# Performance work log

Measured on AMD Instinct MI355X. Metric: run time of the kernel, lower is better.

Reference implementation:

```python
import jax, jax.numpy as jnp
import numpy as np

B, T, D = 8, 1024, 1024
H, HD, KVH, R = 16, 64, 4, 256   # heads, head_dim, kv_heads, kv_lora_rank
K = 31                            # depthwise conv kernel
FF = 4 * D
EPS = 1e-5


def _ln(x, g, b):
    m = jnp.mean(x, -1, keepdims=True)
    v = jnp.mean((x - m) ** 2, -1, keepdims=True)
    return (x - m) * jax.lax.rsqrt(v + EPS) * g + b


def _rope_tables(seq, dim):
    inv = 1.0 / (10000.0 ** (np.arange(0, dim, 2, dtype=np.float32) / dim))
    t = np.arange(seq, dtype=np.float32)
    f = np.einsum('i,j->ij', t, inv)
    emb = np.concatenate([f, f], -1)
    return jnp.asarray(np.cos(emb)), jnp.asarray(np.sin(emb))


def _rope(x, cos, sin):
    # x: [B, h, T, HD]; cos/sin: [T, HD]
    x1, x2 = jnp.split(x, 2, axis=-1)
    return x * cos + jnp.concatenate([-x2, x1], -1) * sin


def setup_inputs() -> dict:
    key = jax.random.key(0)
    ks = iter(jax.random.split(key, 48))
    def w(shape, s=0.02):
        return jax.random.normal(next(ks), shape, jnp.float32) * s
    d = {}
    d['x'] = jax.random.normal(next(ks), (B, T, D), jnp.float32)
    d['ff1_ng'] = jnp.ones(D); d['ff1_nb'] = jnp.zeros(D)
    d['ff1_w1'] = w((D, FF)); d['ff1_b1'] = jnp.zeros(FF)
    d['ff1_w2'] = w((FF, D)); d['ff1_b2'] = jnp.zeros(D)
    d['attn_ng'] = jnp.ones(D); d['attn_nb'] = jnp.zeros(D)
    d['wq'] = w((D, H * HD)); d['wkva'] = w((D, R + HD))
    d['kvn_g'] = jnp.ones(R); d['kvn_b'] = jnp.zeros(R)
    d['wkvb'] = w((R, KVH * HD * 2)); d['wo'] = w((H * HD, D))
    d['conv_ng'] = jnp.ones(D); d['conv_nb'] = jnp.zeros(D)
    d['pw1_w'] = w((D, 2 * D)); d['pw1_b'] = jnp.zeros(2 * D)
    d['dw_w'] = w((D, 1, K)); d['dw_b'] = jnp.zeros(D)
    d['bn_g'] = jnp.ones(D); d['bn_b'] = jnp.zeros(D)
    d['bn_rm'] = jnp.zeros(D); d['bn_rv'] = jnp.ones(D)
    d['pw2_w'] = w((D, D)); d['pw2_b'] = jnp.zeros(D)
    d['ff2_ng'] = jnp.ones(D); d['ff2_nb'] = jnp.zeros(D)
    d['ff2_w1'] = w((D, FF)); d['ff2_b1'] = jnp.zeros(FF)
    d['ff2_w2'] = w((FF, D)); d['ff2_b2'] = jnp.zeros(D)
    d['fin_g'] = jnp.ones(D); d['fin_b'] = jnp.zeros(D)
    return d


def _ffn(x, ng, nb, w1, b1, w2, b2):
    h = jax.nn.silu(_ln(x, ng, nb) @ w1 + b1)
    return h @ w2 + b2


def _rmla(x, ng, nb, wq, wkva, kvn_g, kvn_b, wkvb, wo):
    h = _ln(x, ng, nb)
    q = (h @ wq).reshape(B, T, H, HD).transpose(0, 2, 1, 3)
    kva = h @ wkva                                  # [B,T,R+HD]; k_pe part unused (as in source)
    lat = _ln(kva[..., :R], kvn_g, kvn_b)
    kv = lat @ wkvb
    k = kv[..., :KVH * HD].reshape(B, T, KVH, HD).transpose(0, 2, 1, 3)
    v = kv[..., KVH * HD:].reshape(B, T, KVH, HD).transpose(0, 2, 1, 3)
    cos, sin = _rope_tables(T, HD)
    q = _rope(q, cos, sin)
    k = _rope(k, cos, sin)
    g = H // KVH
    k = jnp.repeat(k, g, axis=1)
    v = jnp.repeat(v, g, axis=1)
    s = jnp.einsum('bhqd,bhkd->bhqk', q, k) * (HD ** -0.5)
    a = jax.nn.softmax(s.astype(jnp.float32), axis=-1).astype(q.dtype)
    o = jnp.einsum('bhqk,bhkd->bhqd', a, v)
    o = o.transpose(0, 2, 1, 3).reshape(B, T, H * HD)
    return o @ wo


def _convmod(x, ng, nb, pw1_w, pw1_b, dw_w, dw_b, bn_g, bn_b, bn_rm, bn_rv, pw2_w, pw2_b):
    h = _ln(x, ng, nb)
    h = h @ pw1_w + pw1_b                           # [B,T,2D]
    a, gate = jnp.split(h, 2, axis=-1)
    h = a * jax.nn.sigmoid(gate)                    # GLU over channels
    h = h.transpose(0, 2, 1)                        # [B,D,T]
    h = jax.lax.conv_general_dilated(h, dw_w, (1,), [(K // 2, K // 2)],
                                     dimension_numbers=('NCH', 'OIH', 'NCH'),
                                     feature_group_count=D) + dw_b[None, :, None]
    h = (h - bn_rm[None, :, None]) * jax.lax.rsqrt(bn_rv[None, :, None] + EPS)
    h = h * bn_g[None, :, None] + bn_b[None, :, None]
    h = jax.nn.silu(h)
    h = h.transpose(0, 2, 1)                        # [B,T,D]
    return h @ pw2_w + pw2_b


def reference(x, ff1_ng, ff1_nb, ff1_w1, ff1_b1, ff1_w2, ff1_b2,
              attn_ng, attn_nb, wq, wkva, kvn_g, kvn_b, wkvb, wo,
              conv_ng, conv_nb, pw1_w, pw1_b, dw_w, dw_b, bn_g, bn_b, bn_rm, bn_rv, pw2_w, pw2_b,
              ff2_ng, ff2_nb, ff2_w1, ff2_b1, ff2_w2, ff2_b2, fin_g, fin_b):
    # Conformer block (macaron): half-FF, RMLA attention, gated depthwise conv, half-FF, final LN
    x = x + 0.5 * _ffn(x, ff1_ng, ff1_nb, ff1_w1, ff1_b1, ff1_w2, ff1_b2)
    x = x + _rmla(x, attn_ng, attn_nb, wq, wkva, kvn_g, kvn_b, wkvb, wo)
    x = x + _convmod(x, conv_ng, conv_nb, pw1_w, pw1_b, dw_w, dw_b, bn_g, bn_b, bn_rm, bn_rv, pw2_w, pw2_b)
    x = x + 0.5 * _ffn(x, ff2_ng, ff2_nb, ff2_w1, ff2_b1, ff2_w2, ff2_b2)
    return _ln(x, fin_g, fin_b)
```

## Files before the change

kernel.cpp:

```cpp
#include <hip/hip_runtime.h>
#include <stdint.h>

typedef unsigned short u16;
using bf16x8 = __attribute__((ext_vector_type(8))) __bf16;
using f32x4  = __attribute__((ext_vector_type(4))) float;

__device__ __forceinline__ u16 f2bf(float f) {
    uint32_t u = __float_as_uint(f);
    u += 0x7fffu + ((u >> 16) & 1u);
    return (u16)(u >> 16);
}
__device__ __forceinline__ float bf2f(u16 u) {
    return __uint_as_float(((uint32_t)u) << 16);
}
__device__ __forceinline__ void gload16(const void* g, void* l) {
    __builtin_amdgcn_global_load_lds(
        (__attribute__((address_space(1))) void*)(uintptr_t)g,
        (__attribute__((address_space(3))) void*)(uintptr_t)l,
        16, 0, 0);
}

template <int OUTF32>
__global__ __launch_bounds__(256) void ln_kernel(const float* __restrict__ in,
                                                 const float* __restrict__ g,
                                                 const float* __restrict__ b,
                                                 void* __restrict__ out, int D) {
    const int row = blockIdx.x;
    const int tid = threadIdx.x;
    const float* x = in + (size_t)row * D;
    const int nv = D >> 8;
    float v[4];
    float s1 = 0.f, s2 = 0.f;
    for (int i = 0; i < nv; ++i) {
        float t = x[tid + (i << 8)];
        v[i] = t; s1 += t; s2 += t * t;
    }
    for (int o = 1; o < 64; o <<= 1) {
        s1 += __shfl_xor(s1, o, 64);
        s2 += __shfl_xor(s2, o, 64);
    }
    __shared__ float r1[4], r2[4];
    const int w = tid >> 6;
    if ((tid & 63) == 0) { r1[w] = s1; r2[w] = s2; }
    __syncthreads();
    s1 = r1[0] + r1[1] + r1[2] + r1[3];
    s2 = r2[0] + r2[1] + r2[2] + r2[3];
    const float mean = s1 / (float)D;
    const float var  = s2 / (float)D - mean * mean;
    const float inv  = rsqrtf(var + 1e-5f);
    for (int i = 0; i < nv; ++i) {
        int c = tid + (i << 8);
        float y = (v[i] - mean) * inv * g[c] + b[c];
        if (OUTF32) ((float*)out)[(size_t)row * D + c] = y;
        else        ((u16*)out)[(size_t)row * D + c] = f2bf(y);
    }
}

template <int GLUPERM>
__global__ __launch_bounds__(256) void wconvert_t(const float* __restrict__ W,
                                                  u16* __restrict__ Wt,
                                                  int K, int N, int ldw) {
    __shared__ float tile[32][33];
    const int k0 = blockIdx.x * 32, n0 = blockIdx.y * 32;
    const int tx = threadIdx.x & 31, ty = threadIdx.x >> 5;
    const int csrc = GLUPERM ? ((tx & 1) * 1024 + (n0 >> 1) + (tx >> 1)) : (n0 + tx);
    for (int i = 0; i < 4; ++i)
        tile[ty + i * 8][tx] = W[(size_t)(k0 + ty + i * 8) * ldw + csrc];
    __syncthreads();
    for (int i = 0; i < 4; ++i)
        Wt[(size_t)(n0 + ty + i * 8) * K + k0 + tx] = f2bf(tile[tx][ty + i * 8]);
}

template <int EPI>
__global__ __launch_bounds__(256) void gemm_bf16(const u16* __restrict__ A,
                                                 const u16* __restrict__ Bt,
                                                 const float* __restrict__ bias,
                                                 const float* __restrict__ res,
                                                 float rscale,
                                                 void* __restrict__ outp,
                                                 int M, int N, int K, int nbx) {
    __shared__ u16 sA[128 * 64];
    __shared__ u16 sB[128 * 64];
    const int tid = threadIdx.x;
    const int lane = tid & 63;
    const int w = tid >> 6;
    const int wm = w >> 1, wn = w & 1;
    const int fr = lane & 15, fq = lane >> 4, frx = fr & 7;
    const int cpx = gridDim.x >> 3;
    const int lid = (blockIdx.x & 7) * cpx + (blockIdx.x >> 3);
    const int bn0 = (lid % nbx) * 128;
    const int bm0 = (lid / nbx) * 128;

    f32x4 acc[4][4] = {};

    const int lrow = lane >> 3;
    const int lslot = (lane & 7) ^ lrow;
    const u16* ga0 = A  + (size_t)(bm0 + w * 8 + lrow) * K + lslot * 8;
    const u16* gb0 = Bt + (size_t)(bn0 + w * 8 + lrow) * K + lslot * 8;
    u16* la0 = sA + w * 512;
    u16* lb0 = sB + w * 512;
    const size_t rstep32 = (size_t)32 * K;

    for (int kt = 0; kt < K; kt += 64) {
        __syncthreads();
#pragma unroll
        for (int i = 0; i < 4; ++i) {
            gload16(ga0 + kt + i * rstep32, la0 + i * 2048);
            gload16(gb0 + kt + i * rstep32, lb0 + i * 2048);
        }
        __syncthreads();
#pragma unroll
        for (int kk = 0; kk < 2; ++kk) {
            bf16x8 afr[4], bfr[4];
            const int sl = (((kk * 4 + fq) ^ frx) << 3);
#pragma unroll
            for (int i = 0; i < 4; ++i) {
                afr[i] = *(const bf16x8*)(sA + (wm * 64 + i * 16 + fr) * 64 + sl);
                bfr[i] = *(const bf16x8*)(sB + (wn * 64 + i * 16 + fr) * 64 + sl);
            }
#pragma unroll
            for (int mi = 0; mi < 4; ++mi)
#pragma unroll
                for (int ni = 0; ni < 4; ++ni)
                    acc[mi][ni] = __builtin_amdgcn_mfma_f32_16x16x32_bf16(
                        bfr[ni], afr[mi], acc[mi][ni], 0, 0, 0);
        }
    }

#pragma unroll
    for (int mi = 0; mi < 4; ++mi) {
        const int m = bm0 + wm * 64 + mi * 16 + fr;
#pragma unroll
        for (int ni = 0; ni < 4; ++ni) {
            const int n0 = bn0 + wn * 64 + ni * 16 + fq * 4;
            if (EPI == 0 || EPI == 1) {
                union { uint2 u2; u16 hh[4]; } ok;
#pragma unroll
                for (int r = 0; r < 4; ++r) {
                    float v = acc[mi][ni][r] + (bias ? bias[n0 + r] : 0.f);
                    if (EPI == 1) v = v / (1.f + __expf(-v));
                    ok.hh[r] = f2bf(v);
                }
                *(uint2*)((u16*)outp + (size_t)m * N + n0) = ok.u2;
            } else if (EPI == 2) {
                f32x4 v;
#pragma unroll
                for (int r = 0; r < 4; ++r)
                    v[r] = acc[mi][ni][r] + (bias ? bias[n0 + r] : 0.f);
                *(f32x4*)((float*)outp + (size_t)m * N + n0) = v;
            } else if (EPI == 3) {
                const f32x4 rv = *(const f32x4*)(res + (size_t)m * N + n0);
                f32x4 v;
#pragma unroll
                for (int r = 0; r < 4; ++r)
                    v[r] = rv[r] + rscale * (acc[mi][ni][r] + (bias ? bias[n0 + r] : 0.f));
                *(f32x4*)((float*)outp + (size_t)m * N + n0) = v;
            } else {
                float vv[4];
#pragma unroll
                for (int r = 0; r < 4; ++r) {
                    const int n = n0 + r;
                    vv[r] = acc[mi][ni][r] + bias[((n & 1) << 10) + (n >> 1)];
                }
                union { uint32_t u; u16 hh[2]; } ok;
                ok.hh[0] = f2bf(vv[0] / (1.f + __expf(-vv[1])));
                ok.hh[1] = f2bf(vv[2] / (1.f + __expf(-vv[3])));
                *(uint32_t*)((u16*)outp + (size_t)m * (N >> 1) + (n0 >> 1)) = ok.u;
            }
        }
    }
}

__global__ __launch_bounds__(256) void rope_tables_kernel(float* __restrict__ ct,
                                                          float* __restrict__ st) {
    const int i = blockIdx.x * 256 + threadIdx.x;
    const int t = i >> 5, j = i & 31;
    const float inv = powf(10000.f, -(float)j / 32.f);
    const float f = (float)t * inv;
    ct[i] = cosf(f);
    st[i] = sinf(f);
}

__global__ __launch_bounds__(256) void rope_kernel(u16* __restrict__ buf,
                                                   const float* __restrict__ ct,
                                                   const float* __restrict__ st,
                                                   int hmask, int hshift, int rstride,
                                                   float scale) {
    const int i = blockIdx.x * 256 + threadIdx.x;
    const int j = i & 31;
    const int hh = (i >> 5) & hmask;
    const int m = i >> (5 + hshift);
    const int t = m & 1023;
    u16* p = buf + (size_t)m * rstride + hh * 64 + j;
    const float c = ct[t * 32 + j], s = st[t * 32 + j];
    const float x1 = bf2f(p[0]), x2 = bf2f(p[32]);
    p[0]  = f2bf((x1 * c - x2 * s) * scale);
    p[32] = f2bf((x2 * c + x1 * s) * scale);
}

__global__ __launch_bounds__(256) void vtranspose_kernel(const u16* __restrict__ KV,
                                                         u16* __restrict__ Vt) {
    __shared__ u16 tile[32][33];
    const int t0 = blockIdx.x * 32, h0 = blockIdx.y * 32;
    const int bk = blockIdx.z;
    const int b = bk >> 2, kh = bk & 3;
    const int tx = threadIdx.x & 31, ty = threadIdx.x >> 5;
    for (int i = 0; i < 4; ++i)
        tile[ty + i * 8][tx] =
            KV[(size_t)(b * 1024 + t0 + ty + i * 8) * 512 + 256 + kh * 64 + h0 + tx];
    __syncthreads();
    for (int i = 0; i < 4; ++i)
        Vt[((size_t)bk * 64 + h0 + ty + i * 8) * 1024 + t0 + tx] = tile[tx][ty + i * 8];
}

__global__ __launch_bounds__(256) void attn_kernel(const u16* __restrict__ Q,
                                                   const u16* __restrict__ KV,
                                                   const u16* __restrict__ Vt,
                                                   u16* __restrict__ O) {
    __shared__ __align__(16) u16 sK[2][64 * 64];
    __shared__ __align__(16) u16 sV[2][64 * 64];
    __shared__ __align__(16) u16 sP[4][16 * 64];
    const int tid = threadIdx.x, lane = tid & 63, w = tid >> 6;
    const int fr = lane & 15, fq = lane >> 4, frx = fr & 7;
    const int bk = blockIdx.x, b = bk >> 2, kh = bk & 3;
    const int h = kh * 4 + w;
    const int q0 = blockIdx.y * 16;
    const int qrow = b * 1024 + q0 + fr;

    const int srow = w * 16 + (lane >> 3);
    const int sslot = (lane & 7) ^ ((lane >> 3) & 7);
    const u16* gK = KV + (size_t)(b * 1024 + srow) * 512 + kh * 64 + sslot * 8;
    const u16* gV = Vt + (size_t)((b * 4 + kh) * 64 + srow) * 1024 + sslot * 8;
    u16* dK = (u16*)sK + w * 16 * 64;
    u16* dV = (u16*)sV + w * 16 * 64;

    bf16x8 qf[2];
    qf[0] = *(const bf16x8*)(Q + (size_t)qrow * 1024 + h * 64 + fq * 8);
    qf[1] = *(const bf16x8*)(Q + (size_t)qrow * 1024 + h * 64 + 32 + fq * 8);

    f32x4 oacc[4] = {};
    float mrun = -1e30f, lrun = 0.f;
    u16* sPw = sP[w];

    gload16(gK, dK);
    gload16(gK + (size_t)8 * 512, dK + 8 * 64);
    gload16(gV, dV);
    gload16(gV + (size_t)8 * 1024, dV + 8 * 64);
    __syncthreads();

    int cur = 0;
    for (int t = 0; t < 16; ++t) {
        const int kv0 = t * 64;
        if (t < 15) {
            const int kn = kv0 + 64;
            const int nx = (cur ^ 1) * 4096;
            gload16(gK + (size_t)kn * 512,       dK + nx);
            gload16(gK + (size_t)(kn + 8) * 512, dK + nx + 8 * 64);
            gload16(gV + kn,                     dV + nx);
            gload16(gV + kn + (size_t)8 * 1024,  dV + nx + 8 * 64);
        }
        const u16* sKc = (u16*)sK + cur * 4096;
        const u16* sVc = (u16*)sV + cur * 4096;
        f32x4 sacc[4] = {};
#pragma unroll
        for (int ks = 0; ks < 2; ++ks)
#pragma unroll
            for (int nb = 0; nb < 4; ++nb) {
                const bf16x8 kf = *(const bf16x8*)(
                    sKc + (nb * 16 + fr) * 64 + (((ks * 4 + fq) ^ frx) << 3));
                sacc[nb] = __builtin_amdgcn_mfma_f32_16x16x32_bf16(kf, qf[ks], sacc[nb], 0, 0, 0);
            }
        float pm;
        {
            float a0 = fmaxf(fmaxf(sacc[0][0], sacc[0][1]), fmaxf(sacc[0][2], sacc[0][3]));
            float a1 = fmaxf(fmaxf(sacc[1][0], sacc[1][1]), fmaxf(sacc[1][2], sacc[1][3]));
            float a2 = fmaxf(fmaxf(sacc[2][0], sacc[2][1]), fmaxf(sacc[2][2], sacc[2][3]));
            float a3 = fmaxf(fmaxf(sacc[3][0], sacc[3][1]), fmaxf(sacc[3][2], sacc[3][3]));
            pm = fmaxf(fmaxf(a0, a1), fmaxf(a2, a3));
        }
        pm = fmaxf(pm, __shfl_xor(pm, 16, 64));
        pm = fmaxf(pm, __shfl_xor(pm, 32, 64));
        if (!__all(pm <= mrun + 8.f)) {
            const float mn = fmaxf(mrun, pm);
            const float al = __expf(mrun - mn);
            mrun = mn;
            lrun *= al;
#pragma unroll
            for (int f = 0; f < 4; ++f) {
                f32x4 tt = oacc[f];
#pragma unroll
                for (int r = 0; r < 4; ++r) tt[r] *= al;
                oacc[f] = tt;
            }
        }
        float rs = 0.f;
#pragma unroll
        for (int nb = 0; nb < 4; ++nb) {
            union { uint2 u2; u16 hh[4]; } pk;
#pragma unroll
            for (int r = 0; r < 4; ++r) {
                const float p = __expf(sacc[nb][r] - mrun);
                rs += p;
                pk.hh[r] = f2bf(p);
            }
            const int slotl = nb * 2 + (fq >> 1);
            *(uint2*)(sPw + fr * 64 + (((slotl ^ frx) << 3) | ((fq & 1) << 2))) = pk.u2;
        }
        rs += __shfl_xor(rs, 16, 64);
        rs += __shfl_xor(rs, 32, 64);
        lrun += rs;
        asm volatile("s_waitcnt lgkmcnt(0)" ::: "memory");
        __builtin_amdgcn_sched_barrier(0);
#pragma unroll
        for (int ks2 = 0; ks2 < 2; ++ks2) {
            const bf16x8 pf = *(const bf16x8*)(
                sPw + fr * 64 + (((ks2 * 4 + fq) ^ frx) << 3));
#pragma unroll
            for (int f = 0; f < 4; ++f) {
                const bf16x8 vf = *(const bf16x8*)(
                    sVc + (f * 16 + fr) * 64 + (((ks2 * 4 + fq) ^ frx) << 3));
                oacc[f] = __builtin_amdgcn_mfma_f32_16x16x32_bf16(vf, pf, oacc[f], 0, 0, 0);
            }
        }
        __syncthreads();
        cur ^= 1;
    }

    const float linv = 1.f / lrun;
#pragma unroll
    for (int f = 0; f < 4; ++f) {
        union { uint2 u2; u16 hh[4]; } ok;
#pragma unroll
        for (int r = 0; r < 4; ++r) ok.hh[r] = f2bf(oacc[f][r] * linv);
        *(uint2*)(O + (size_t)qrow * 1024 + h * 64 + f * 16 + fq * 4) = ok.u2;
    }
}

__global__ __launch_bounds__(256) void dwconv_kernel(const u16* __restrict__ G,
                                                     const float* __restrict__ wt,
                                                     const float* __restrict__ wb,
                                                     const float* __restrict__ bg,
                                                     const float* __restrict__ bb,
                                                     const float* __restrict__ rm,
                                                     const float* __restrict__ rv,
                                                     u16* __restrict__ out) {
    __shared__ u16 sg[38 * 256];
    const int tid = threadIdx.x;
    const int d = blockIdx.x * 256 + tid;
    const int t0 = blockIdx.y * 8;
    const int b = blockIdx.z;
    const size_t base = (size_t)b * 1024 * 1024 + d;
    for (int i = 0; i < 38; ++i) {
        const int t = t0 - 15 + i;
        sg[i * 256 + tid] = (t >= 0 && t < 1024) ? G[base + (size_t)t * 1024] : (u16)0;
    }
    __syncthreads();
    float wreg[31];
#pragma unroll
    for (int k = 0; k < 31; ++k) wreg[k] = wt[d * 31 + k];
    const float scale = bg[d] * rsqrtf(rv[d] + 1e-5f);
    const float addv = wb[d] - rm[d];
#pragma unroll
    for (int j = 0; j < 8; ++j) {
        float acc = 0.f;
#pragma unroll
        for (int k = 0; k < 31; ++k) acc += bf2f(sg[(j + k) * 256 + tid]) * wreg[k];
        float y = (acc + addv) * scale + bb[d];
        y = y / (1.f + __expf(-y));
        out[base + (size_t)(t0 + j) * 1024] = f2bf(y);
    }
}

extern "C" void kernel_launch(void* const* d_in, const int* in_sizes, int n_in,
                              void* d_out, int out_size, void* d_ws, size_t ws_size,
                              hipStream_t stream) {
    (void)in_sizes; (void)n_in; (void)out_size;

    const float* x       = (const float*)d_in[0];
    const float* ff1_ng  = (const float*)d_in[1];
    const float* ff1_nb  = (const float*)d_in[2];
    const float* ff1_w1  = (const float*)d_in[3];
    const float* ff1_b1  = (const float*)d_in[4];
    const float* ff1_w2  = (const float*)d_in[5];
    const float* ff1_b2  = (const float*)d_in[6];
    const float* attn_ng = (const float*)d_in[7];
    const float* attn_nb = (const float*)d_in[8];
    const float* wq      = (const float*)d_in[9];
    const float* wkva    = (const float*)d_in[10];
    const float* kvn_g   = (const float*)d_in[11];
    const float* kvn_b   = (const float*)d_in[12];
    const float* wkvb    = (const float*)d_in[13];
    const float* wo      = (const float*)d_in[14];
    const float* conv_ng = (const float*)d_in[15];
    const float* conv_nb = (const float*)d_in[16];
    const float* pw1_w   = (const float*)d_in[17];
    const float* pw1_b   = (const float*)d_in[18];
    const float* dw_w    = (const float*)d_in[19];
    const float* dw_b    = (const float*)d_in[20];
    const float* bn_g    = (const float*)d_in[21];
    const float* bn_b    = (const float*)d_in[22];
    const float* bn_rm   = (const float*)d_in[23];
    const float* bn_rv   = (const float*)d_in[24];
    const float* pw2_w   = (const float*)d_in[25];
    const float* pw2_b   = (const float*)d_in[26];
    const float* ff2_ng  = (const float*)d_in[27];
    const float* ff2_nb  = (const float*)d_in[28];
    const float* ff2_w1  = (const float*)d_in[29];
    const float* ff2_b1  = (const float*)d_in[30];
    const float* ff2_w2  = (const float*)d_in[31];
    const float* ff2_b2  = (const float*)d_in[32];
    const float* fin_g   = (const float*)d_in[33];
    const float* fin_b   = (const float*)d_in[34];

    const int M = 8192;
    char* ws = (char*)d_ws;
    size_t off = 0;
    auto alloc = [&](size_t bytes) {
        size_t o = off;
        off += (bytes + 255) & ~(size_t)255;
        return o;
    };
    const size_t o_ff1w1 = alloc((size_t)4096 * 1024 * 2);
    const size_t o_ff1w2 = alloc((size_t)1024 * 4096 * 2);
    const size_t o_wq    = alloc((size_t)1024 * 1024 * 2);
    const size_t o_wkva  = alloc((size_t)256 * 1024 * 2);
    const size_t o_wkvb  = alloc((size_t)512 * 256 * 2);
    const size_t o_wo    = alloc((size_t)1024 * 1024 * 2);
    const size_t o_pw1   = alloc((size_t)2048 * 1024 * 2);
    const size_t o_pw2   = alloc((size_t)1024 * 1024 * 2);
    const size_t o_ff2w1 = alloc((size_t)4096 * 1024 * 2);
    const size_t o_ff2w2 = alloc((size_t)1024 * 4096 * 2);
    const size_t o_ctab  = alloc((size_t)1024 * 32 * 4);
    const size_t o_stab  = alloc((size_t)1024 * 32 * 4);
    const size_t o_xres  = alloc((size_t)M * 1024 * 4);
    const size_t o_ln    = alloc((size_t)M * 1024 * 2);
    const size_t o_bufa  = alloc((size_t)64 * 1024 * 1024);
    if (ws_size < off) return;

    u16* BUFA = (u16*)(ws + o_bufa);
    u16* Qb    = BUFA;
    u16* KVb   = (u16*)((char*)BUFA + (16u << 20));
    float* KVA = (float*)((char*)BUFA + (24u << 20));
    u16* LAT   = (u16*)((char*)BUFA + (32u << 20));
    u16* VT    = (u16*)((char*)BUFA + (36u << 20));
    u16* OB    = (u16*)((char*)BUFA + (40u << 20));
    u16* PW1G  = BUFA;
    u16* CONVO = (u16*)((char*)BUFA + (16u << 20));
    u16* HID   = BUFA;

    u16* WT_FF1W1 = (u16*)(ws + o_ff1w1);
    u16* WT_FF1W2 = (u16*)(ws + o_ff1w2);
    u16* WT_WQ    = (u16*)(ws + o_wq);
    u16* WT_WKVA  = (u16*)(ws + o_wkva);
    u16* WT_WKVB  = (u16*)(ws + o_wkvb);
    u16* WT_WO    = (u16*)(ws + o_wo);
    u16* WT_PW1   = (u16*)(ws + o_pw1);
    u16* WT_PW2   = (u16*)(ws + o_pw2);
    u16* WT_FF2W1 = (u16*)(ws + o_ff2w1);
    u16* WT_FF2W2 = (u16*)(ws + o_ff2w2);
    float* CT = (float*)(ws + o_ctab);
    float* ST = (float*)(ws + o_stab);
    float* XR = (float*)(ws + o_xres);
    u16* LNB  = (u16*)(ws + o_ln);

    wconvert_t<0><<<dim3(32, 128), 256, 0, stream>>>(ff1_w1, WT_FF1W1, 1024, 4096, 4096);
    wconvert_t<0><<<dim3(128, 32), 256, 0, stream>>>(ff1_w2, WT_FF1W2, 4096, 1024, 1024);
    wconvert_t<0><<<dim3(32, 32),  256, 0, stream>>>(wq,     WT_WQ,    1024, 1024, 1024);
    wconvert_t<0><<<dim3(32, 8),   256, 0, stream>>>(wkva,   WT_WKVA,  1024, 256,  320);
    wconvert_t<0><<<dim3(8, 16),   256, 0, stream>>>(wkvb,   WT_WKVB,  256,  512,  512);
    wconvert_t<0><<<dim3(32, 32),  256, 0, stream>>>(wo,     WT_WO,    1024, 1024, 1024);
    wconvert_t<1><<<dim3(32, 64),  256, 0, stream>>>(pw1_w,  WT_PW1,   1024, 2048, 2048);
    wconvert_t<0><<<dim3(32, 32),  256, 0, stream>>>(pw2_w,  WT_PW2,   1024, 1024, 1024);
    wconvert_t<0><<<dim3(32, 128), 256, 0, stream>>>(ff2_w1, WT_FF2W1, 1024, 4096, 4096);
    wconvert_t<0><<<dim3(128, 32), 256, 0, stream>>>(ff2_w2, WT_FF2W2, 4096, 1024, 1024);
    rope_tables_kernel<<<128, 256, 0, stream>>>(CT, ST);

    ln_kernel<0><<<M, 256, 0, stream>>>(x, ff1_ng, ff1_nb, LNB, 1024);
    gemm_bf16<1><<<2048, 256, 0, stream>>>(LNB, WT_FF1W1, ff1_b1, nullptr, 0.f, HID, M, 4096, 1024, 32);
    gemm_bf16<3><<<512, 256, 0, stream>>>(HID, WT_FF1W2, ff1_b2, x, 0.5f, XR, M, 1024, 4096, 8);

    ln_kernel<0><<<M, 256, 0, stream>>>(XR, attn_ng, attn_nb, LNB, 1024);
    gemm_bf16<0><<<512, 256, 0, stream>>>(LNB, WT_WQ, nullptr, nullptr, 0.f, Qb, M, 1024, 1024, 8);
    gemm_bf16<2><<<128, 256, 0, stream>>>(LNB, WT_WKVA, nullptr, nullptr, 0.f, KVA, M, 256, 1024, 2);
    ln_kernel<0><<<M, 256, 0, stream>>>(KVA, kvn_g, kvn_b, LAT, 256);
    gemm_bf16<0><<<256, 256, 0, stream>>>(LAT, WT_WKVB, nullptr, nullptr, 0.f, KVb, M, 512, 256, 4);
    rope_kernel<<<16384, 256, 0, stream>>>(Qb, CT, ST, 15, 4, 1024, 0.125f);
    rope_kernel<<<4096, 256, 0, stream>>>(KVb, CT, ST, 3, 2, 512, 1.0f);
    vtranspose_kernel<<<dim3(32, 2, 32), 256, 0, stream>>>(KVb, VT);
    attn_kernel<<<dim3(32, 64), 256, 0, stream>>>(Qb, KVb, VT, OB);
    gemm_bf16<3><<<512, 256, 0, stream>>>(OB, WT_WO, nullptr, XR, 1.f, XR, M, 1024, 1024, 8);

    ln_kernel<0><<<M, 256, 0, stream>>>(XR, conv_ng, conv_nb, LNB, 1024);
    gemm_bf16<4><<<1024, 256, 0, stream>>>(LNB, WT_PW1, pw1_b, nullptr, 0.f, PW1G, M, 2048, 1024, 16);
    dwconv_kernel<<<dim3(4, 128, 8), 256, 0, stream>>>(PW1G, dw_w, dw_b, bn_g, bn_b, bn_rm, bn_rv, CONVO);
    gemm_bf16<3><<<512, 256, 0, stream>>>(CONVO, WT_PW2, pw2_b, XR, 1.f, XR, M, 1024, 1024, 8);

    ln_kernel<0><<<M, 256, 0, stream>>>(XR, ff2_ng, ff2_nb, LNB, 1024);
    gemm_bf16<1><<<2048, 256, 0, stream>>>(LNB, WT_FF2W1, ff2_b1, nullptr, 0.f, HID, M, 4096, 1024, 32);
    gemm_bf16<3><<<512, 256, 0, stream>>>(HID, WT_FF2W2, ff2_b2, XR, 0.5f, XR, M, 1024, 4096, 8);

    ln_kernel<1><<<M, 256, 0, stream>>>(XR, fin_g, fin_b, d_out, 1024);
}
```

Baseline: 809.9 us.

## Double-buffer GEMM mainloop, fuse RoPE into projection epilogues, batch weight conversions

```diff
diff --git a/kernel.cpp b/kernel.cpp
--- a/kernel.cpp
+++ b/kernel.cpp
@@ -57,9 +57,13 @@
 }
 
 template <int GLUPERM>
-__global__ __launch_bounds__(256) void wconvert_t(const float* __restrict__ W,
-                                                  u16* __restrict__ Wt,
+__global__ __launch_bounds__(256) void wconvert_t(const float* __restrict__ W0,
+                                                  u16* __restrict__ Wt0,
+                                                  const float* __restrict__ W1,
+                                                  u16* __restrict__ Wt1,
                                                   int K, int N, int ldw) {
+    const float* W = blockIdx.z ? W1 : W0;
+    u16* Wt = blockIdx.z ? Wt1 : Wt0;
     __shared__ float tile[32][33];
     const int k0 = blockIdx.x * 32, n0 = blockIdx.y * 32;
     const int tx = threadIdx.x & 31, ty = threadIdx.x >> 5;
@@ -72,18 +76,18 @@
 }
 
 template <int EPI>
-__global__ __launch_bounds__(256) void gemm_bf16(const u16* __restrict__ A,
-                                                 const u16* __restrict__ Bt,
-                                                 const float* __restrict__ bias,
-                                                 const float* __restrict__ res,
-                                                 float rscale,
-                                                 void* __restrict__ outp,
-                                                 int M, int N, int K, int nbx) {
-    __shared__ u16 sA[128 * 64];
-    __shared__ u16 sB[128 * 64];
-    const int tid = threadIdx.x;
-    const int lane = tid & 63;
-    const int w = tid >> 6;
+__global__ __launch_bounds__(256, 2) void gemm128p(const u16* __restrict__ A,
+                                                   const u16* __restrict__ Bt,
+                                                   const float* __restrict__ bias,
+                                                   const float* __restrict__ res,
+                                                   float rscale,
+                                                   void* __restrict__ outp,
+                                                   const float* __restrict__ CT,
+                                                   const float* __restrict__ ST,
+                                                   int M, int N, int K, int nbx) {
+    __shared__ u16 sA[2][128 * 64];
+    __shared__ u16 sB[2][128 * 64];
+    const int tid = threadIdx.x, lane = tid & 63, w = tid >> 6;
     const int wm = w >> 1, wn = w & 1;
     const int fr = lane & 15, fq = lane >> 4, frx = fr & 7;
     const int cpx = gridDim.x >> 3;
@@ -97,39 +101,103 @@
     const int lslot = (lane & 7) ^ lrow;
     const u16* ga0 = A  + (size_t)(bm0 + w * 8 + lrow) * K + lslot * 8;
     const u16* gb0 = Bt + (size_t)(bn0 + w * 8 + lrow) * K + lslot * 8;
-    u16* la0 = sA + w * 512;
-    u16* lb0 = sB + w * 512;
     const size_t rstep32 = (size_t)32 * K;
-
-    for (int kt = 0; kt < K; kt += 64) {
-        __syncthreads();
+    const int NK = K >> 6;
+
+#define STAGE(bufi, kt)                                                         \
+    {                                                                           \
+        _Pragma("unroll")                                                       \
+        for (int i = 0; i < 4; ++i) {                                           \
+            gload16(ga0 + (kt) + i * rstep32, &sA[bufi][w * 512 + i * 2048]);   \
+            gload16(gb0 + (kt) + i * rstep32, &sB[bufi][w * 512 + i * 2048]);   \
+        }                                                                       \
+    }
+#define SB() __builtin_amdgcn_sched_barrier(0)
+
+    STAGE(0, 0)
+    STAGE(1, 64)
+    asm volatile("s_waitcnt vmcnt(8)" ::: "memory");
+    SB();
+    __builtin_amdgcn_s_barrier();
+
+    for (int s = 0; s < NK; ++s) {
+        const int buf = s & 1;
+        bf16x8 afr[4], bfr[4], afr2[4], bfr2[4];
 #pragma unroll
         for (int i = 0; i < 4; ++i) {
-            gload16(ga0 + kt + i * rstep32, la0 + i * 2048);
-            gload16(gb0 + kt + i * rstep32, lb0 + i * 2048);
-        }
-        __syncthreads();
-#pragma unroll
-        for (int kk = 0; kk < 2; ++kk) {
-            bf16x8 afr[4], bfr[4];
-            const int sl = (((kk * 4 + fq) ^ frx) << 3);
-#pragma unroll
-            for (int i = 0; i < 4; ++i) {
-                afr[i] = *(const bf16x8*)(sA + (wm * 64 + i * 16 + fr) * 64 + sl);
-                bfr[i] = *(const bf16x8*)(sB + (wn * 64 + i * 16 + fr) * 64 + sl);
-            }
-#pragma unroll
-            for (int mi = 0; mi < 4; ++mi)
-#pragma unroll
-                for (int ni = 0; ni < 4; ++ni)
-                    acc[mi][ni] = __builtin_amdgcn_mfma_f32_16x16x32_bf16(
-                        bfr[ni], afr[mi], acc[mi][ni], 0, 0, 0);
-        }
+            afr[i] = *(const bf16x8*)(&sA[buf][(wm * 64 + i * 16 + fr) * 64 + ((fq ^ frx) << 3)]);
+            bfr[i] = *(const bf16x8*)(&sB[buf][(wn * 64 + i * 16 + fr) * 64 + ((fq ^ frx) << 3)]);
+        }
+        asm volatile("s_waitcnt lgkmcnt(0)" ::: "memory");
+        SB();
+        __builtin_amdgcn_s_setprio(1);
+#pragma unroll
+        for (int mi = 0; mi < 4; ++mi)
+#pragma unroll
+            for (int ni = 0; ni < 4; ++ni)
+                acc[mi][ni] = __builtin_amdgcn_mfma_f32_16x16x32_bf16(
+                    bfr[ni], afr[mi], acc[mi][ni], 0, 0, 0);
+        __builtin_amdgcn_s_setprio(0);
+#pragma unroll
+        for (int i = 0; i < 4; ++i) {
+            afr2[i] = *(const bf16x8*)(&sA[buf][(wm * 64 + i * 16 + fr) * 64 + (((4 + fq) ^ frx) << 3)]);
+            bfr2[i] = *(const bf16x8*)(&sB[buf][(wn * 64 + i * 16 + fr) * 64 + (((4 + fq) ^ frx) << 3)]);
+        }
+        asm volatile("s_waitcnt lgkmcnt(0)" ::: "memory");
+        SB();
+        __builtin_amdgcn_s_barrier();
+        if (s + 2 < NK) STAGE(buf, (s + 2) << 6)
+        SB();
+        __builtin_amdgcn_s_setprio(1);
+#pragma unroll
+        for (int mi = 0; mi < 4; ++mi)
+#pragma unroll
+            for (int ni = 0; ni < 4; ++ni)
+                acc[mi][ni] = __builtin_amdgcn_mfma_f32_16x16x32_bf16(
+                    bfr2[ni], afr2[mi], acc[mi][ni], 0, 0, 0);
+        __builtin_amdgcn_s_setprio(0);
+        if (s + 2 < NK) { asm volatile("s_waitcnt vmcnt(8)" ::: "memory"); }
+        else            { asm volatile("s_waitcnt vmcnt(0)" ::: "memory"); }
+        SB();
+        __builtin_amdgcn_s_barrier();
     }
 
 #pragma unroll
     for (int mi = 0; mi < 4; ++mi) {
         const int m = bm0 + wm * 64 + mi * 16 + fr;
+        if (EPI == 5 || EPI == 6) {
+            const int t = m & 1023;
+            const int colbase = bn0 + wn * 64;
+            const bool dorope = (EPI == 5) || (colbase < 256);
+            if (dorope) {
+#pragma unroll
+                for (int ni = 0; ni < 2; ++ni) {
+                    const int j0 = ni * 16 + fq * 4;
+                    const f32x4 c = *(const f32x4*)(CT + t * 32 + j0);
+                    const f32x4 sn = *(const f32x4*)(ST + t * 32 + j0);
+                    union { uint2 u2; u16 hh[4]; } o1, o2;
+#pragma unroll
+                    for (int r = 0; r < 4; ++r) {
+                        const float x1 = acc[mi][ni][r];
+                        const float x2 = acc[mi][ni + 2][r];
+                        o1.hh[r] = f2bf((x1 * c[r] - x2 * sn[r]) * rscale);
+                        o2.hh[r] = f2bf((x2 * c[r] + x1 * sn[r]) * rscale);
+                    }
+                    *(uint2*)((u16*)outp + (size_t)m * N + colbase + j0) = o1.u2;
+                    *(uint2*)((u16*)outp + (size_t)m * N + colbase + j0 + 32) = o2.u2;
+                }
+            } else {
+#pragma unroll
+                for (int ni = 0; ni < 4; ++ni) {
+                    const int n0 = colbase + ni * 16 + fq * 4;
+                    union { uint2 u2; u16 hh[4]; } ok;
+#pragma unroll
+                    for (int r = 0; r < 4; ++r) ok.hh[r] = f2bf(acc[mi][ni][r]);
+                    *(uint2*)((u16*)outp + (size_t)m * N + n0) = ok.u2;
+                }
+            }
+            continue;
+        }
 #pragma unroll
         for (int ni = 0; ni < 4; ++ni) {
             const int n0 = bn0 + wn * 64 + ni * 16 + fq * 4;
@@ -155,7 +223,7 @@
                 for (int r = 0; r < 4; ++r)
                     v[r] = rv[r] + rscale * (acc[mi][ni][r] + (bias ? bias[n0 + r] : 0.f));
                 *(f32x4*)((float*)outp + (size_t)m * N + n0) = v;
-            } else {
+            } else if (EPI == 4) {
                 float vv[4];
 #pragma unroll
                 for (int r = 0; r < 4; ++r) {
@@ -169,6 +237,8 @@
             }
         }
     }
+#undef STAGE
+#undef SB
 }
 
 __global__ __launch_bounds__(256) void rope_tables_kernel(float* __restrict__ ct,
@@ -179,23 +249,6 @@
     const float f = (float)t * inv;
     ct[i] = cosf(f);
     st[i] = sinf(f);
-}
-
-__global__ __launch_bounds__(256) void rope_kernel(u16* __restrict__ buf,
-                                                   const float* __restrict__ ct,
-                                                   const float* __restrict__ st,
-                                                   int hmask, int hshift, int rstride,
-                                                   float scale) {
-    const int i = blockIdx.x * 256 + threadIdx.x;
-    const int j = i & 31;
-    const int hh = (i >> 5) & hmask;
-    const int m = i >> (5 + hshift);
-    const int t = m & 1023;
-    u16* p = buf + (size_t)m * rstride + hh * 64 + j;
-    const float c = ct[t * 32 + j], s = st[t * 32 + j];
-    const float x1 = bf2f(p[0]), x2 = bf2f(p[32]);
-    p[0]  = f2bf((x1 * c - x2 * s) * scale);
-    p[32] = f2bf((x2 * c + x1 * s) * scale);
 }
 
 __global__ __launch_bounds__(256) void vtranspose_kernel(const u16* __restrict__ KV,
@@ -463,41 +516,36 @@
     float* XR = (float*)(ws + o_xres);
     u16* LNB  = (u16*)(ws + o_ln);
 
-    wconvert_t<0><<<dim3(32, 128), 256, 0, stream>>>(ff1_w1, WT_FF1W1, 1024, 4096, 4096);
-    wconvert_t<0><<<dim3(128, 32), 256, 0, stream>>>(ff1_w2, WT_FF1W2, 4096, 1024, 1024);
-    wconvert_t<0><<<dim3(32, 32),  256, 0, stream>>>(wq,     WT_WQ,    1024, 1024, 1024);
-    wconvert_t<0><<<dim3(32, 8),   256, 0, stream>>>(wkva,   WT_WKVA,  1024, 256,  320);
-    wconvert_t<0><<<dim3(8, 16),   256, 0, stream>>>(wkvb,   WT_WKVB,  256,  512,  512);
-    wconvert_t<0><<<dim3(32, 32),  256, 0, stream>>>(wo,     WT_WO,    1024, 1024, 1024);
-    wconvert_t<1><<<dim3(32, 64),  256, 0, stream>>>(pw1_w,  WT_PW1,   1024, 2048, 2048);
-    wconvert_t<0><<<dim3(32, 32),  256, 0, stream>>>(pw2_w,  WT_PW2,   1024, 1024, 1024);
-    wconvert_t<0><<<dim3(32, 128), 256, 0, stream>>>(ff2_w1, WT_FF2W1, 1024, 4096, 4096);
-    wconvert_t<0><<<dim3(128, 32), 256, 0, stream>>>(ff2_w2, WT_FF2W2, 4096, 1024, 1024);
+    wconvert_t<0><<<dim3(32, 128, 2), 256, 0, stream>>>(ff1_w1, WT_FF1W1, ff2_w1, WT_FF2W1, 1024, 4096, 4096);
+    wconvert_t<0><<<dim3(128, 32, 2), 256, 0, stream>>>(ff1_w2, WT_FF1W2, ff2_w2, WT_FF2W2, 4096, 1024, 1024);
+    wconvert_t<0><<<dim3(32, 32, 2),  256, 0, stream>>>(wq, WT_WQ, wo, WT_WO, 1024, 1024, 1024);
+    wconvert_t<0><<<dim3(32, 32, 1),  256, 0, stream>>>(pw2_w, WT_PW2, pw2_w, WT_PW2, 1024, 1024, 1024);
+    wconvert_t<0><<<dim3(32, 8, 1),   256, 0, stream>>>(wkva, WT_WKVA, wkva, WT_WKVA, 1024, 256, 320);
+    wconvert_t<0><<<dim3(8, 16, 1),   256, 0, stream>>>(wkvb, WT_WKVB, wkvb, WT_WKVB, 256, 512, 512);
+    wconvert_t<1><<<dim3(32, 64, 1),  256, 0, stream>>>(pw1_w, WT_PW1, pw1_w, WT_PW1, 1024, 2048, 2048);
     rope_tables_kernel<<<128, 256, 0, stream>>>(CT, ST);
 
     ln_kernel<0><<<M, 256, 0, stream>>>(x, ff1_ng, ff1_nb, LNB, 1024);
-    gemm_bf16<1><<<2048, 256, 0, stream>>>(LNB, WT_FF1W1, ff1_b1, nullptr, 0.f, HID, M, 4096, 1024, 32);
-    gemm_bf16<3><<<512, 256, 0, stream>>>(HID, WT_FF1W2, ff1_b2, x, 0.5f, XR, M, 1024, 4096, 8);
+    gemm128p<1><<<2048, 256, 0, stream>>>(LNB, WT_FF1W1, ff1_b1, nullptr, 0.f, HID, nullptr, nullptr, M, 4096, 1024, 32);
+    gemm128p<3><<<512, 256, 0, stream>>>(HID, WT_FF1W2, ff1_b2, x, 0.5f, XR, nullptr, nullptr, M, 1024, 4096, 8);
 
     ln_kernel<0><<<M, 256, 0, stream>>>(XR, attn_ng, attn_nb, LNB, 1024);
-    gemm_bf16<0><<<512, 256, 0, stream>>>(LNB, WT_WQ, nullptr, nullptr, 0.f, Qb, M, 1024, 1024, 8);
-    gemm_bf16<2><<<128, 256, 0, stream>>>(LNB, WT_WKVA, nullptr, nullptr, 0.f, KVA, M, 256, 1024, 2);
+    gemm128p<5><<<512, 256, 0, stream>>>(LNB, WT_WQ, nullptr, nullptr, 0.125f, Qb, CT, ST, M, 1024, 1024, 8);
+    gemm128p<2><<<128, 256, 0, stream>>>(LNB, WT_WKVA, nullptr, nullptr, 0.f, KVA, nullptr, nullptr, M, 256, 1024, 2);
     ln_kernel<0><<<M, 256, 0, stream>>>(KVA, kvn_g, kvn_b, LAT, 256);
-    gemm_bf16<0><<<256, 256, 0, stream>>>(LAT, WT_WKVB, nullptr, nullptr, 0.f, KVb, M, 512, 256, 4);
-    rope_kernel<<<16384, 256, 0, stream>>>(Qb, CT, ST, 15, 4, 1024, 0.125f);
-    rope_kernel<<<4096, 256, 0, stream>>>(KVb, CT, ST, 3, 2, 512, 1.0f);
+    gemm128p<6><<<256, 256, 0, stream>>>(LAT, WT_WKVB, nullptr, nullptr, 1.0f, KVb, CT, ST, M, 512, 256, 4);
     vtranspose_kernel<<<dim3(32, 2, 32), 256, 0, stream>>>(KVb, VT);
     attn_kernel<<<dim3(32, 64), 256, 0, stream>>>(Qb, KVb, VT, OB);
-    gemm_bf16<3><<<512, 256, 0, stream>>>(OB, WT_WO, nullptr, XR, 1.f, XR, M, 1024, 1024, 8);
+    gemm128p<3><<<512, 256, 0, stream>>>(OB, WT_WO, nullptr, XR, 1.f, XR, nullptr, nullptr, M, 1024, 1024, 8);
 
     ln_kernel<0><<<M, 256, 0, stream>>>(XR, conv_ng, conv_nb, LNB, 1024);
-    gemm_bf16<4><<<1024, 256, 0, stream>>>(LNB, WT_PW1, pw1_b, nullptr, 0.f, PW1G, M, 2048, 1024, 16);
+    gemm128p<4><<<1024, 256, 0, stream>>>(LNB, WT_PW1, pw1_b, nullptr, 0.f, PW1G, nullptr, nullptr, M, 2048, 1024, 16);
     dwconv_kernel<<<dim3(4, 128, 8), 256, 0, stream>>>(PW1G, dw_w, dw_b, bn_g, bn_b, bn_rm, bn_rv, CONVO);
-    gemm_bf16<3><<<512, 256, 0, stream>>>(CONVO, WT_PW2, pw2_b, XR, 1.f, XR, M, 1024, 1024, 8);
+    gemm128p<3><<<512, 256, 0, stream>>>(CONVO, WT_PW2, pw2_b, XR, 1.f, XR, nullptr, nullptr, M, 1024, 1024, 8);
 
     ln_kernel<0><<<M, 256, 0, stream>>>(XR, ff2_ng, ff2_nb, LNB, 1024);
-    gemm_bf16<1><<<2048, 256, 0, stream>>>(LNB, WT_FF2W1, ff2_b1, nullptr, 0.f, HID, M, 4096, 1024, 32);
-    gemm_bf16<3><<<512, 256, 0, stream>>>(HID, WT_FF2W2, ff2_b2, XR, 0.5f, XR, M, 1024, 4096, 8);
+    gemm128p<1><<<2048, 256, 0, stream>>>(LNB, WT_FF2W1, ff2_b1, nullptr, 0.f, HID, nullptr, nullptr, M, 4096, 1024, 32);
+    gemm128p<3><<<512, 256, 0, stream>>>(HID, WT_FF2W2, ff2_b2, XR, 0.5f, XR, nullptr, nullptr, M, 1024, 4096, 8);
 
     ln_kernel<1><<<M, 256, 0, stream>>>(XR, fin_g, fin_b, d_out, 1024);
 }
```

After: 771.5 us. 1.05x faster.
